# Optimization experiments

Measured on AMD Instinct MI355X. Metric: run time of the kernel, lower is better.

The kernel has to match this reference:

```python
import jax, jax.numpy as jnp
import numpy as np

D_SCALED = 8  # adaptive pool output spatial size


def setup_inputs() -> dict:
    key = jax.random.key(0)
    ks = jax.random.split(key, 5)
    b, t, c, h, w = 8, 16, 64, 56, 56
    d_t = 16
    d_in = D_SCALED * D_SCALED  # 64
    d_out = d_t * 2             # 32
    return {
        "x": jax.random.normal(ks[0], (b, t, c, h, w), dtype=jnp.float32),
        "Wq": jax.random.normal(ks[1], (d_in, d_out), dtype=jnp.float32) * 0.001,
        "bq": jax.random.normal(ks[2], (d_out,), dtype=jnp.float32) * 0.001,
        "Wk": jax.random.normal(ks[3], (d_in, d_out), dtype=jnp.float32) * 0.001,
        "bk": jax.random.normal(ks[4], (d_out,), dtype=jnp.float32) * 0.001,
    }


def reference(x, Wq, bq, Wk, bk):
    b, t, c, h, w = x.shape
    ds = D_SCALED
    # shift_x: [b, c, t, h, w]
    shift = jnp.transpose(x, (0, 2, 1, 3, 4))
    # AdaptiveAvgPool3d((None, ds, ds)): h,w divide evenly -> reshape-mean
    pooled = shift.reshape(b, c, t, ds, h // ds, ds, w // ds).mean(axis=(4, 6))
    flat = pooled.reshape(b * c, t, ds * ds)          # [bc, t, ds*ds]
    q = flat @ Wq + bq                                # [bc, t, 2*d_t]
    k = flat @ Wk + bk                                # [bc, t, 2*d_t]
    att = jnp.einsum('ntd,nsd->nts', q, k) / np.sqrt(t).astype(jnp.float32)
    att = jax.nn.softmax(att, axis=-1)                # [bc, t, t]
    v = shift.reshape(b * c, t, h * w)                # [bc, t, h*w]
    out = jnp.einsum('nts,nsv->ntv', att, v)          # [bc, t, h*w]
    out = out.reshape(b, c, t, h, w)
    return jnp.transpose(out, (0, 2, 1, 3, 4))        # [b, t, c, h, w]
```

## Files before the change

kernel.cpp:

```cpp
#include <hip/hip_runtime.h>
#include <math.h>

#define B  8
#define T  16
#define C  64
#define H  56
#define W  56
#define HW (H*W)
#define HW4 (HW/4)
#define DS 8
#define DIN (DS*DS)
#define DOUT 32
#define BC (B*C)

typedef float vfloat4 __attribute__((ext_vector_type(4)));


__global__ __launch_bounds__(256) void pool_kernel(const float* __restrict__ x,
                                                   float* __restrict__ pooled_g) {
    __shared__ float xs[HW];
    __shared__ float part[256];
    const int n = blockIdx.x;
    const int t = blockIdx.y;
    const int tid = threadIdx.x;
    const int b = n >> 6;
    const int c = n & 63;

    const float4* x4 = (const float4*)x;
    float4* xs4 = (float4*)xs;
    const size_t base = ((size_t)(b * T + t) * C + c) * HW4;

    for (int i = tid; i < HW4; i += 256) xs4[i] = x4[base + i];
    __syncthreads();

    {
        const int wi = tid & 63;
        const int q  = tid >> 6;
        const int ri = wi >> 3;
        const int rj = wi & 7;
        const int r0 = 2 * q;
        const int nrows = (q < 3) ? 2 : 1;
        float s = 0.f;
        for (int dr = 0; dr < nrows; ++dr) {
            const int row = 7 * ri + r0 + dr;
            const int col0 = 7 * rj;
            #pragma unroll
            for (int dj = 0; dj < 7; ++dj) s += xs[row * W + col0 + dj];
        }
        part[q * 64 + wi] = s;
    }
    __syncthreads();

    if (tid < 64) {
        const float v = part[tid] + part[tid + 64] + part[tid + 128] + part[tid + 192];
        pooled_g[((size_t)n * T + t) * DIN + tid] = v * (1.0f / 49.0f);
    }
}

__global__ __launch_bounds__(256) void att_kernel(const float* __restrict__ pooled_g,
                                                  const float* __restrict__ Wq,
                                                  const float* __restrict__ bq,
                                                  const float* __restrict__ Wk,
                                                  const float* __restrict__ bk,
                                                  float* __restrict__ att_g) {
    __shared__ float pooled_s[T * DIN];
    __shared__ float qs[T * 33];
    __shared__ float ks[T * 33];
    __shared__ float att_s[T * T];

    const int n = blockIdx.x;
    const int tid = threadIdx.x;

    for (int e = tid; e < T * DIN; e += 256) pooled_s[e] = pooled_g[(size_t)n * (T * DIN) + e];
    __syncthreads();

    for (int e = tid; e < T * DOUT; e += 256) {
        const int t = e >> 5;
        const int d = e & 31;
        float sq = bq[d];
        float sk = bk[d];
        #pragma unroll 8
        for (int kk = 0; kk < DIN; ++kk) {
            const float f = pooled_s[t * DIN + kk];
            sq = fmaf(f, Wq[kk * DOUT + d], sq);
            sk = fmaf(f, Wk[kk * DOUT + d], sk);
        }
        qs[t * 33 + d] = sq;
        ks[t * 33 + d] = sk;
    }
    __syncthreads();

    {
        const int tt = tid >> 4;
        const int ss = tid & 15;
        float s = 0.f;
        #pragma unroll
        for (int d = 0; d < DOUT; ++d) s = fmaf(qs[tt * 33 + d], ks[ss * 33 + d], s);
        att_s[tid] = s * 0.25f;
    }
    __syncthreads();

    if (tid < T) {
        const int r = tid;
        float m = -INFINITY;
        #pragma unroll
        for (int s = 0; s < T; ++s) m = fmaxf(m, att_s[r * T + s]);
        float e[T];
        float sum = 0.f;
        #pragma unroll
        for (int s = 0; s < T; ++s) { e[s] = __expf(att_s[r * T + s] - m); sum += e[s]; }
        const float inv = 1.0f / sum;
        #pragma unroll
        for (int s = 0; s < T; ++s) att_g[(size_t)n * (T * T) + r * T + s] = e[s] * inv;
    }
}

__global__ __launch_bounds__(128) void apply_kernel(const float* __restrict__ x,
                                                    const float* __restrict__ att_g,
                                                    float* __restrict__ out) {
    __shared__ float att_s[T * T];
    const int n = blockIdx.x;
    const int chunk = blockIdx.y;
    const int tid = threadIdx.x;
    const int lane = tid & 63;
    const int wave = tid >> 6;
    const int b = n >> 6;
    const int c = n & 63;

    for (int e = tid; e < T * T; e += 128) att_s[e] = att_g[(size_t)n * (T * T) + e];
    __syncthreads();

    const float4* x4 = (const float4*)x;
    float4* o4 = (float4*)out;

    #pragma unroll 1
    for (int i = lane; i < 112; i += 64) {
        const int p4 = chunk * 112 + i;
        float4 acc[8];
        #pragma unroll
        for (int t = 0; t < 8; ++t) acc[t] = make_float4(0.f, 0.f, 0.f, 0.f);

        #pragma unroll 8
        for (int s = 0; s < T; ++s) {
            const float4 xv = x4[((size_t)(b * T + s) * C + c) * HW4 + p4];
            #pragma unroll
            for (int t = 0; t < 8; ++t) {
                const float a = att_s[(wave * 8 + t) * T + s];
                acc[t].x = fmaf(a, xv.x, acc[t].x);
                acc[t].y = fmaf(a, xv.y, acc[t].y);
                acc[t].z = fmaf(a, xv.z, acc[t].z);
                acc[t].w = fmaf(a, xv.w, acc[t].w);
            }
        }

        #pragma unroll
        for (int t = 0; t < 8; ++t) {
            vfloat4* dst = (vfloat4*)&o4[((size_t)(b * T + wave * 8 + t) * C + c) * HW4 + p4];
            vfloat4 v; v.x = acc[t].x; v.y = acc[t].y; v.z = acc[t].z; v.w = acc[t].w;
            __builtin_nontemporal_store(v, dst);
        }
    }
}

extern "C" void kernel_launch(void* const* d_in, const int* in_sizes, int n_in,
                              void* d_out, int out_size, void* d_ws, size_t ws_size,
                              hipStream_t stream) {
    const float* x  = (const float*)d_in[0];
    const float* Wq = (const float*)d_in[1];
    const float* bq = (const float*)d_in[2];
    const float* Wk = (const float*)d_in[3];
    const float* bk = (const float*)d_in[4];
    float* out = (float*)d_out;

    float* pooled_g = out;
    float* att_g = (float*)d_ws;

    pool_kernel<<<dim3(BC, T), dim3(256), 0, stream>>>(x, pooled_g);
    att_kernel<<<dim3(BC), dim3(256), 0, stream>>>(pooled_g, Wq, bq, Wk, bk, att_g);
    apply_kernel<<<dim3(BC, 7), dim3(128), 0, stream>>>(x, att_g, out);
}
```

Before: 211.7 us.

## Restructure apply kernel into one 1024-thread block per channel with transposed attention

The attention matrix is now stored transposed, so each apply step reads two float4 attention vectors from LDS instead of eight scalars. The apply kernel becomes one 1024-thread block per (b,c), replacing 7 chunks of 128 threads. Two halves of the block each produce 8 output time steps over all columns, and stores are plain instead of nontemporal. This cuts grid size and LDS traffic but changes the occupancy and wave scheduling of a kernel that is bound by memory bandwidth.

```diff
diff --git a/kernel.cpp b/kernel.cpp
--- a/kernel.cpp
+++ b/kernel.cpp
@@ -111,53 +111,81 @@
         for (int s = 0; s < T; ++s) { e[s] = __expf(att_s[r * T + s] - m); sum += e[s]; }
         const float inv = 1.0f / sum;
         #pragma unroll
-        for (int s = 0; s < T; ++s) att_g[(size_t)n * (T * T) + r * T + s] = e[s] * inv;
-    }
-}
-
-__global__ __launch_bounds__(128) void apply_kernel(const float* __restrict__ x,
-                                                    const float* __restrict__ att_g,
-                                                    float* __restrict__ out) {
-    __shared__ float att_s[T * T];
+        for (int s = 0; s < T; ++s) att_g[(size_t)n * (T * T) + s * T + r] = e[s] * inv;
+    }
+}
+
+__global__ __launch_bounds__(1024, 4) void apply_kernel(const float* __restrict__ x,
+                                                        const float* __restrict__ att_g,
+                                                        float* __restrict__ out) {
+    __shared__ float att_lds[T * T];
     const int n = blockIdx.x;
-    const int chunk = blockIdx.y;
     const int tid = threadIdx.x;
-    const int lane = tid & 63;
-    const int wave = tid >> 6;
     const int b = n >> 6;
     const int c = n & 63;
 
-    for (int e = tid; e < T * T; e += 128) att_s[e] = att_g[(size_t)n * (T * T) + e];
-    __syncthreads();
+    if (tid < 256) att_lds[tid] = att_g[(size_t)n * 256 + tid];
+    __syncthreads();
+
+    const int half  = tid >> 9;
+    const int inner = tid & 511;
+    const int q0 = half * 2;
+    const float4* att4 = (const float4*)att_lds;
 
     const float4* x4 = (const float4*)x;
     float4* o4 = (float4*)out;
+    const size_t base = ((size_t)(b * T) * C + c) * HW4;
+    const size_t tstr = (size_t)C * HW4;
 
     #pragma unroll 1
-    for (int i = lane; i < 112; i += 64) {
-        const int p4 = chunk * 112 + i;
+    for (int col = inner; col < HW4; col += 512) {
         float4 acc[8];
         #pragma unroll
-        for (int t = 0; t < 8; ++t) acc[t] = make_float4(0.f, 0.f, 0.f, 0.f);
-
-        #pragma unroll 8
+        for (int j = 0; j < 8; ++j) acc[j] = make_float4(0.f, 0.f, 0.f, 0.f);
+
+        #pragma unroll 2
         for (int s = 0; s < T; ++s) {
-            const float4 xv = x4[((size_t)(b * T + s) * C + c) * HW4 + p4];
-            #pragma unroll
-            for (int t = 0; t < 8; ++t) {
-                const float a = att_s[(wave * 8 + t) * T + s];
-                acc[t].x = fmaf(a, xv.x, acc[t].x);
-                acc[t].y = fmaf(a, xv.y, acc[t].y);
-                acc[t].z = fmaf(a, xv.z, acc[t].z);
-                acc[t].w = fmaf(a, xv.w, acc[t].w);
-            }
-        }
-
-        #pragma unroll
-        for (int t = 0; t < 8; ++t) {
-            vfloat4* dst = (vfloat4*)&o4[((size_t)(b * T + wave * 8 + t) * C + c) * HW4 + p4];
-            vfloat4 v; v.x = acc[t].x; v.y = acc[t].y; v.z = acc[t].z; v.w = acc[t].w;
-            __builtin_nontemporal_store(v, dst);
+            const float4 xv = x4[base + (size_t)s * tstr + col];
+            const float4 a0 = att4[s * 4 + q0];
+            const float4 a1 = att4[s * 4 + q0 + 1];
+            acc[0].x = fmaf(a0.x, xv.x, acc[0].x);
+            acc[0].y = fmaf(a0.x, xv.y, acc[0].y);
+            acc[0].z = fmaf(a0.x, xv.z, acc[0].z);
+            acc[0].w = fmaf(a0.x, xv.w, acc[0].w);
+            acc[1].x = fmaf(a0.y, xv.x, acc[1].x);
+            acc[1].y = fmaf(a0.y, xv.y, acc[1].y);
+            acc[1].z = fmaf(a0.y, xv.z, acc[1].z);
+            acc[1].w = fmaf(a0.y, xv.w, acc[1].w);
+            acc[2].x = fmaf(a0.z, xv.x, acc[2].x);
+            acc[2].y = fmaf(a0.z, xv.y, acc[2].y);
+            acc[2].z = fmaf(a0.z, xv.z, acc[2].z);
+            acc[2].w = fmaf(a0.z, xv.w, acc[2].w);
+            acc[3].x = fmaf(a0.w, xv.x, acc[3].x);
+            acc[3].y = fmaf(a0.w, xv.y, acc[3].y);
+            acc[3].z = fmaf(a0.w, xv.z, acc[3].z);
+            acc[3].w = fmaf(a0.w, xv.w, acc[3].w);
+            acc[4].x = fmaf(a1.x, xv.x, acc[4].x);
+            acc[4].y = fmaf(a1.x, xv.y, acc[4].y);
+            acc[4].z = fmaf(a1.x, xv.z, acc[4].z);
+            acc[4].w = fmaf(a1.x, xv.w, acc[4].w);
+            acc[5].x = fmaf(a1.y, xv.x, acc[5].x);
+            acc[5].y = fmaf(a1.y, xv.y, acc[5].y);
+            acc[5].z = fmaf(a1.y, xv.z, acc[5].z);
+            acc[5].w = fmaf(a1.y, xv.w, acc[5].w);
+            acc[6].x = fmaf(a1.z, xv.x, acc[6].x);
+            acc[6].y = fmaf(a1.z, xv.y, acc[6].y);
+            acc[6].z = fmaf(a1.z, xv.z, acc[6].z);
+            acc[6].w = fmaf(a1.z, xv.w, acc[6].w);
+            acc[7].x = fmaf(a1.w, xv.x, acc[7].x);
+            acc[7].y = fmaf(a1.w, xv.y, acc[7].y);
+            acc[7].z = fmaf(a1.w, xv.z, acc[7].z);
+            acc[7].w = fmaf(a1.w, xv.w, acc[7].w);
+        }
+
+        #pragma unroll
+        for (int j = 0; j < 8; ++j) {
+            const int t = half * 8 + j;
+            o4[base + (size_t)t * tstr + col] = acc[j];
         }
     }
 }
@@ -177,5 +205,5 @@
 
     pool_kernel<<<dim3(BC, T), dim3(256), 0, stream>>>(x, pooled_g);
     att_kernel<<<dim3(BC), dim3(256), 0, stream>>>(pooled_g, Wq, bq, Wk, bk, att_g);
-    apply_kernel<<<dim3(BC, 7), dim3(128), 0, stream>>>(x, att_g, out);
-}
+    apply_kernel<<<dim3(BC), dim3(1024), 0, stream>>>(x, att_g, out);
+}
```

After: 213.3 us. Within noise of the previous version (+0.8%).
